# Optimization experiments

Measured on AMD Instinct MI355X. Metric: run time of the kernel, lower is better.

Reference implementation:

```python
import jax, jax.numpy as jnp
import numpy as np

EPS = 1e-5
NUM_HEADS = 8
KEY_DIM = 16
D = 64  # attn_ratio * key_dim


def conv1x1_bn(x, w, g, b, m, v):
    # x: (B, Cin, H, W), w: (Cout, Cin); eval-mode BatchNorm over channel dim
    y = jnp.einsum('bchw,oc->bohw', x, w)
    scale = (g * jax.lax.rsqrt(v + EPS))[None, :, None, None]
    shift = (b - g * m * jax.lax.rsqrt(v + EPS))[None, :, None, None]
    return y * scale + shift


def setup_inputs() -> dict:
    key = jax.random.key(0)
    ks = jax.random.split(key, 22)
    dim, nh_kd, dh = 384, 128, 512
    f = jax.random.normal
    u = jax.random.uniform
    return {
        'x': f(ks[0], (2, dim, 56, 56), jnp.float32),
        'wq': f(ks[1], (nh_kd, dim), jnp.float32) * 0.05,
        'qg': u(ks[2], (nh_kd,), jnp.float32), 'qb': f(ks[3], (nh_kd,)) * 0.1,
        'qm': f(ks[4], (nh_kd,)) * 0.1, 'qv': u(ks[5], (nh_kd,)) + 0.5,
        'wk': f(ks[6], (nh_kd, dim), jnp.float32) * 0.05,
        'kg': u(ks[7], (nh_kd,), jnp.float32), 'kb': f(ks[8], (nh_kd,)) * 0.1,
        'km': f(ks[9], (nh_kd,)) * 0.1, 'kvv': u(ks[10], (nh_kd,)) + 0.5,
        'wv': f(ks[11], (dh, dim), jnp.float32) * 0.05,
        'vg': u(ks[12], (dh,), jnp.float32), 'vb': f(ks[13], (dh,)) * 0.1,
        'vm': f(ks[14], (dh,)) * 0.1, 'vvv': u(ks[15], (dh,)) + 0.5,
        'wp': f(ks[16], (dim, dh), jnp.float32) * 0.05,
        'pg': u(ks[17], (dim,), jnp.float32), 'pb': f(ks[18], (dim,)) * 0.1,
        'pm': f(ks[19], (dim,)) * 0.1, 'pvv': u(ks[20], (dim,)) + 0.5,
    }


def reference(x, wq, qg, qb, qm, qv, wk, kg, kb, km, kvv,
              wv, vg, vb, vm, vvv, wp, pg, pb, pm, pvv):
    B, C, H, W = x.shape
    N = H * W
    h, kd, d = NUM_HEADS, KEY_DIM, D
    # (B, h, N, kd)
    qq = conv1x1_bn(x, wq, qg, qb, qm, qv).reshape(B, h, kd, N).transpose(0, 1, 3, 2)
    # (B, h, kd, N)
    kk = conv1x1_bn(x, wk, kg, kb, km, kvv).reshape(B, h, kd, N)
    # (B, h, N, d)
    vv = conv1x1_bn(x, wv, vg, vb, vm, vvv).reshape(B, h, d, N).transpose(0, 1, 3, 2)
    # NOTE: original forward does NOT apply self.scale
    attn = jax.nn.softmax(jnp.matmul(qq, kk), axis=-1)  # (B, h, N, N)
    xx = jnp.matmul(attn, vv)                            # (B, h, N, d)
    xx = xx.transpose(0, 1, 3, 2).reshape(B, h * d, H, W)
    xx = jax.nn.relu(xx)
    return conv1x1_bn(xx, wp, pg, pb, pm, pvv)
```

## Files before the change

kernel.cpp:

```cpp
#include <hip/hip_runtime.h>
#include <hip/hip_bf16.h>

#define B_   2
#define CIN  384
#define NPIX 3136
#define NH   8
#define KD   16
#define DHEAD 64
#define NHKD 128
#define QKW  256
#define DHD  512
#define EPSW 1e-5f

typedef __attribute__((ext_vector_type(8))) short vshort8;
typedef __attribute__((ext_vector_type(4))) short vshort4;
typedef __attribute__((ext_vector_type(4))) float vfloat4;
typedef __attribute__((ext_vector_type(16))) float vfloat16;

static __device__ __forceinline__ float bf2f(short s) {
    unsigned int u = ((unsigned int)(unsigned short)s) << 16;
    return __builtin_bit_cast(float, u);
}
static __device__ __forceinline__ short f2bf(float f) {
    unsigned int u = __builtin_bit_cast(unsigned int, f);
    unsigned int lsb = (u >> 16) & 1u;
    u += 0x7fffu + lsb;
    return (short)(u >> 16);
}
static __device__ __forceinline__ float pget(const void* p, int i, int f32) {
    return f32 ? ((const float*)p)[i] : bf2f(((const short*)p)[i]);
}

static __device__ __forceinline__ int detect_f32(const unsigned short* x) {
    int lane = threadIdx.x & 63;
    bool big = false;
#pragma unroll
    for (int j = 0; j < 8; j++) {
        int e = (x[(lane * 8 + j) * 2] >> 7) & 0xFF;
        big = big || (e >= 0xC0);
    }
    unsigned long long bal = __ballot(big);
    return __popcll(bal) >= 32;
}

__global__ __launch_bounds__(256) void prep_kernel(
    const void* __restrict__ x,
    const void* __restrict__ wq, const void* __restrict__ wk,
    const void* __restrict__ wv, const void* __restrict__ wp,
    short* __restrict__ wB, short* __restrict__ xT,
    const void* qg, const void* qb, const void* qm, const void* qv,
    const void* kg, const void* kb, const void* km, const void* kv,
    const void* vg, const void* vb, const void* vm, const void* vv,
    const void* pg, const void* pb, const void* pm, const void* pv,
    float* __restrict__ scA, float* __restrict__ shA)
{
    __shared__ short tile[32][33];
    int f32 = detect_f32((const unsigned short*)x);
    int id = blockIdx.x;
    int t = threadIdx.x;

    if (id < 1920) {
        int i = id * 256 + t;
        const void* src; int j;
        if (i < 49152)       { src = wq; j = i; }
        else if (i < 98304)  { src = wk; j = i - 49152; }
        else if (i < 294912) { src = wv; j = i - 98304; }
        else                 { src = wp; j = i - 294912; }
        wB[i] = f32 ? f2bf(((const float*)src)[j]) : ((const short*)src)[j];
        if (i < 1152) {
            const void *g, *bb, *mn, *vr;
            if (i < 128)      { g = qg; bb = qb; mn = qm; vr = qv; j = i; }
            else if (i < 256) { g = kg; bb = kb; mn = km; vr = kv; j = i - 128; }
            else if (i < 768) { g = vg; bb = vb; mn = vm; vr = vv; j = i - 256; }
            else              { g = pg; bb = pb; mn = pm; vr = pv; j = i - 768; }
            float iv = rsqrtf(pget(vr, j, f32) + EPSW);
            float s = pget(g, j, f32) * iv;
            scA[i] = s;
            shA[i] = pget(bb, j, f32) - pget(mn, j, f32) * s;
        }
        return;
    }

    int tid2 = id - 1920;
    int b = tid2 / 1176, rr = tid2 % 1176;
    int n0 = (rr % 98) * 32, c0 = (rr / 98) * 32;
    int r = t >> 3, q4 = (t & 7) * 4;
    size_t off = ((size_t)b * CIN + c0 + r) * NPIX + n0 + q4;
    if (f32) {
        float4 v = *(const float4*)((const float*)x + off);
        tile[r][q4 + 0] = f2bf(v.x);
        tile[r][q4 + 1] = f2bf(v.y);
        tile[r][q4 + 2] = f2bf(v.z);
        tile[r][q4 + 3] = f2bf(v.w);
    } else {
        vshort4 v = *(const vshort4*)((const short*)x + off);
#pragma unroll
        for (int i = 0; i < 4; i++) tile[r][q4 + i] = v[i];
    }
    __syncthreads();
    vshort4 o;
#pragma unroll
    for (int i = 0; i < 4; i++) o[i] = tile[q4 + i][r];
    *(vshort4*)(xT + ((size_t)b * NPIX + n0 + r) * CIN + c0 + q4) = o;
}

static __device__ __forceinline__ void gemm_body(
    short* Al, short* Bl,
    const short* __restrict__ A, const short* __restrict__ Bt,
    void* __restrict__ C, size_t coff, int m0, int n0,
    const float* __restrict__ sc, const float* __restrict__ sh,
    int Nb, int K, int bnPerRow, int finalOut, int f32)
{
    int t = threadIdx.x, lane = t & 63, w = t >> 6, m = lane & 15, quad = lane >> 4;
    int srow = t >> 2, scol = (t & 3) * 16;
    const short* ag = A + (size_t)(m0 + srow) * K + scol;
    const short* bg = Bt + (size_t)(n0 + srow) * K + scol;
    vfloat4 acc[4];
#pragma unroll
    for (int i = 0; i < 4; i++) acc[i] = (vfloat4){0.f, 0.f, 0.f, 0.f};

    for (int k0 = 0; k0 < K; k0 += 64) {
        vshort8 a0 = *(const vshort8*)(ag + k0);
        vshort8 a1 = *(const vshort8*)(ag + k0 + 8);
        vshort8 b0 = *(const vshort8*)(bg + k0);
        vshort8 b1 = *(const vshort8*)(bg + k0 + 8);
        __syncthreads();
        *(vshort8*)&Al[srow * 72 + scol] = a0;
        *(vshort8*)&Al[srow * 72 + scol + 8] = a1;
        *(vshort8*)&Bl[srow * 72 + scol] = b0;
        *(vshort8*)&Bl[srow * 72 + scol + 8] = b1;
        __syncthreads();
#pragma unroll
        for (int kk = 0; kk < 2; kk++) {
            vshort8 af = *(const vshort8*)&Al[(w * 16 + m) * 72 + kk * 32 + quad * 8];
#pragma unroll
            for (int nc = 0; nc < 4; nc++) {
                vshort8 bf = *(const vshort8*)&Bl[(nc * 16 + m) * 72 + kk * 32 + quad * 8];
                acc[nc] = __builtin_amdgcn_mfma_f32_16x16x32_bf16(af, bf, acc[nc], 0, 0, 0);
            }
        }
    }

#pragma unroll
    for (int nc = 0; nc < 4; nc++) {
        int col = n0 + nc * 16 + m;
        float scc = bnPerRow ? 0.f : sc[col];
        float shc = bnPerRow ? 0.f : sh[col];
#pragma unroll
        for (int r = 0; r < 4; r++) {
            int row = m0 + w * 16 + quad * 4 + r;
            float s2 = bnPerRow ? sc[row] : scc;
            float h2 = bnPerRow ? sh[row] : shc;
            float val = s2 * acc[nc][r] + h2;
            size_t idx = coff + (size_t)row * Nb + col;
            if (finalOut && f32) ((float*)C)[idx] = val;
            else                 ((short*)C)[idx] = f2bf(val);
        }
    }
}

__global__ __launch_bounds__(256) void proj_kernel(
    const short* __restrict__ xT, const short* __restrict__ wqkB,
    const short* __restrict__ wvB, short* __restrict__ QKt,
    short* __restrict__ Vb,
    const float* __restrict__ scA, const float* __restrict__ shA)
{
    __shared__ __attribute__((aligned(16))) short Al[64 * 72];
    __shared__ __attribute__((aligned(16))) short Bl[64 * 72];
    int id = blockIdx.x;
    if (id < 392) {
        int b = id / 196, r = id % 196;
        int m0 = (r % 49) * 64, n0 = (r / 49) * 64;
        gemm_body(Al, Bl, xT + (size_t)b * NPIX * CIN, wqkB,
                  QKt, (size_t)b * NPIX * QKW, m0, n0,
                  scA, shA, QKW, CIN, 0, 0, 0);
    } else {
        id -= 392;
        int b = id / 392, r = id % 392;
        int m0 = (r % 8) * 64, n0 = (r / 8) * 64;
        gemm_body(Al, Bl, wvB, xT + (size_t)b * NPIX * CIN,
                  Vb, (size_t)b * DHD * NPIX, m0, n0,
                  scA + 256, shA + 256, NPIX, CIN, 1, 0, 0);
    }
}

__global__ __launch_bounds__(256) void pgemm_kernel(
    const short* __restrict__ wpB, const short* __restrict__ xx,
    void* __restrict__ out,
    const float* __restrict__ scA, const float* __restrict__ shA,
    const void* __restrict__ x)
{
    __shared__ __attribute__((aligned(16))) short Al[64 * 72];
    __shared__ __attribute__((aligned(16))) short Bl[64 * 72];
    int f32 = detect_f32((const unsigned short*)x);
    int id = blockIdx.x;
    int b = id / 294, r = id % 294;
    int m0 = (r % 6) * 64, n0 = (r / 6) * 64;
    gemm_body(Al, Bl, wpB, xx + (size_t)b * NPIX * DHD,
              out, (size_t)b * CIN * NPIX, m0, n0,
              scA + 768, shA + 768, NPIX, DHD, 1, 1, f32);
}

__global__ __launch_bounds__(128) void attn_kernel(
    const short* __restrict__ QKt, const short* __restrict__ V,
    short* __restrict__ xx)
{
    __shared__ __attribute__((aligned(16))) short Kl[2][64 * 16];
    __shared__ __attribute__((aligned(16))) short Vl[2][64 * 72];
    __shared__ __attribute__((aligned(16))) short Pl[64 * 72];
    int bh = blockIdx.y, b = bh >> 3, h = bh & 7;
    int q0 = blockIdx.x * 64;
    int t = threadIdx.x, lane = t & 63, w = t >> 6;
    int c31 = lane & 31, half = lane >> 5;

    int q = q0 + w * 32 + c31;
    vshort8 aq = *(const vshort8*)(QKt + ((size_t)b * NPIX + q) * QKW + h * KD + half * 8);

    vfloat16 o0, o1, oL, z16;
#pragma unroll
    for (int i = 0; i < 16; i++) { o0[i] = 0.f; o1[i] = 0.f; oL[i] = 0.f; z16[i] = 0.f; }

    int kkey = t >> 1, kofs = (t & 1) * 8;
    const short* kgp = QKt + (size_t)b * NPIX * QKW + NHKD + h * KD + kofs;
    int vd = t >> 1, vkh = (t & 1) * 32;
    const short* vgp = V + ((size_t)(b * DHD) + h * DHEAD + vd) * NPIX + vkh;
    const short one_bf = (short)0x3F80;
    const vshort8 ones = {one_bf, one_bf, one_bf, one_bf, one_bf, one_bf, one_bf, one_bf};

    *(vshort8*)&Kl[0][kkey * 16 + kofs] = *(const vshort8*)(kgp + (size_t)kkey * QKW);
#pragma unroll
    for (int i = 0; i < 4; i++)
        *(vshort8*)&Vl[0][vd * 72 + vkh + i * 8] = *(const vshort8*)(vgp + i * 8);
    __syncthreads();

    for (int it = 0; it < NPIX / 64; ++it) {
        int cur = it & 1, nxt = cur ^ 1;
        int k0 = it * 64;
        bool more = (it + 1) < (NPIX / 64);
        vshort8 ks, vs[4];
        if (more) {
            ks = *(const vshort8*)(kgp + (size_t)(k0 + 64 + kkey) * QKW);
#pragma unroll
            for (int i = 0; i < 4; i++)
                vs[i] = *(const vshort8*)(vgp + k0 + 64 + i * 8);
        }

        short* pw = &Pl[(w * 32 + c31) * 72];
#pragma unroll
        for (int kg = 0; kg < 2; kg++) {
            vshort8 ak = *(const vshort8*)&Kl[cur][(kg * 32 + c31) * 16 + half * 8];
            vfloat16 s = __builtin_amdgcn_mfma_f32_32x32x16_bf16(ak, aq, z16, 0, 0, 0);
#pragma unroll
            for (int rb = 0; rb < 4; rb++) {
                vshort4 pv;
#pragma unroll
                for (int j = 0; j < 4; j++) {
                    float p = __expf(s[rb * 4 + j]);
                    pv[j] = (short)(__builtin_bit_cast(unsigned int, p) >> 16);
                }
                *(vshort4*)&pw[kg * 32 + half * 4 + rb * 8] = pv;
            }
        }

#pragma unroll
        for (int kc = 0; kc < 4; kc++) {
            vshort8 ap  = *(const vshort8*)&Pl[(w * 32 + c31) * 72 + kc * 16 + half * 8];
            vshort8 bv0 = *(const vshort8*)&Vl[cur][(c31) * 72 + kc * 16 + half * 8];
            vshort8 bv1 = *(const vshort8*)&Vl[cur][(32 + c31) * 72 + kc * 16 + half * 8];
            o0 = __builtin_amdgcn_mfma_f32_32x32x16_bf16(ap, bv0, o0, 0, 0, 0);
            o1 = __builtin_amdgcn_mfma_f32_32x32x16_bf16(ap, bv1, o1, 0, 0, 0);
            oL = __builtin_amdgcn_mfma_f32_32x32x16_bf16(ap, ones, oL, 0, 0, 0);
        }

        if (more) {
            *(vshort8*)&Kl[nxt][kkey * 16 + kofs] = ks;
#pragma unroll
            for (int i = 0; i < 4; i++)
                *(vshort8*)&Vl[nxt][vd * 72 + vkh + i * 8] = vs[i];
        }
        __syncthreads();
    }

#pragma unroll
    for (int r = 0; r < 16; r++) {
        int ql = (r & 3) + 8 * (r >> 2) + 4 * half;
        int qrow = q0 + w * 32 + ql;
        float inv = 1.0f / oL[r];
        size_t base = ((size_t)b * NPIX + qrow) * DHD + h * DHEAD + c31;
        xx[base]      = f2bf(fmaxf(o0[r] * inv, 0.f));
        xx[base + 32] = f2bf(fmaxf(o1[r] * inv, 0.f));
    }
}

extern "C" void kernel_launch(void* const* d_in, const int* in_sizes, int n_in,
                              void* d_out, int out_size, void* d_ws, size_t ws_size,
                              hipStream_t stream) {
    const void* x  = d_in[0];
    const void* wq = d_in[1];
    const void* qg = d_in[2];  const void* qb = d_in[3];
    const void* qm = d_in[4];  const void* qv = d_in[5];
    const void* wk = d_in[6];
    const void* kg = d_in[7];  const void* kb = d_in[8];
    const void* km = d_in[9];  const void* kv = d_in[10];
    const void* wv = d_in[11];
    const void* vg = d_in[12]; const void* vb = d_in[13];
    const void* vm = d_in[14]; const void* vv = d_in[15];
    const void* wp = d_in[16];
    const void* pg = d_in[17]; const void* pb = d_in[18];
    const void* pm = d_in[19]; const void* pv = d_in[20];

    short* xT  = (short*)d_ws;
    short* wB  = xT + (size_t)B_ * NPIX * CIN;
    short* wqkB = wB;
    short* wvB  = wB + 98304;
    short* wpB  = wB + 294912;
    short* QKt = wB + 491520;
    short* Vb  = QKt + (size_t)B_ * NPIX * QKW;
    short* xx  = Vb + (size_t)B_ * DHD * NPIX;
    float* scA = (float*)(xx + (size_t)B_ * NPIX * DHD);
    float* shA = scA + 1152;

    prep_kernel<<<4272, 256, 0, stream>>>(
        x, wq, wk, wv, wp, wB, xT,
        qg, qb, qm, qv, kg, kb, km, kv,
        vg, vb, vm, vv, pg, pb, pm, pv, scA, shA);

    proj_kernel<<<1176, 256, 0, stream>>>(xT, wqkB, wvB, QKt, Vb, scA, shA);

    attn_kernel<<<dim3(NPIX / 64, B_ * NH), 128, 0, stream>>>(QKt, Vb, xx);

    pgemm_kernel<<<588, 256, 0, stream>>>(wpB, xx, d_out, scA, shA, x);
}
```

Baseline: 197.2 us.

## Retile projection GEMMs to 128x64 with 32x32 MFMA and fold log2e into Q

```diff
diff --git a/kernel.cpp b/kernel.cpp
--- a/kernel.cpp
+++ b/kernel.cpp
@@ -11,11 +11,18 @@
 #define QKW  256
 #define DHD  512
 #define EPSW 1e-5f
+#define L2E  1.4426950408889634f
 
 typedef __attribute__((ext_vector_type(8))) short vshort8;
 typedef __attribute__((ext_vector_type(4))) short vshort4;
 typedef __attribute__((ext_vector_type(4))) float vfloat4;
 typedef __attribute__((ext_vector_type(16))) float vfloat16;
+
+#if __has_builtin(__builtin_amdgcn_exp2f)
+#define EXP2F __builtin_amdgcn_exp2f
+#else
+#define EXP2F exp2f
+#endif
 
 static __device__ __forceinline__ float bf2f(short s) {
     unsigned int u = ((unsigned int)(unsigned short)s) << 16;
@@ -75,8 +82,10 @@
             else              { g = pg; bb = pb; mn = pm; vr = pv; j = i - 768; }
             float iv = rsqrtf(pget(vr, j, f32) + EPSW);
             float s = pget(g, j, f32) * iv;
+            float h = pget(bb, j, f32) - pget(mn, j, f32) * s;
+            if (i < 128) { s *= L2E; h *= L2E; }
             scA[i] = s;
-            shA[i] = pget(bb, j, f32) - pget(mn, j, f32) * s;
+            shA[i] = h;
         }
         return;
     }
@@ -104,54 +113,63 @@
     *(vshort4*)(xT + ((size_t)b * NPIX + n0 + r) * CIN + c0 + q4) = o;
 }
 
-static __device__ __forceinline__ void gemm_body(
+static __device__ __forceinline__ void gemm32_body(
     short* Al, short* Bl,
     const short* __restrict__ A, const short* __restrict__ Bt,
     void* __restrict__ C, size_t coff, int m0, int n0,
     const float* __restrict__ sc, const float* __restrict__ sh,
-    int Nb, int K, int bnPerRow, int finalOut, int f32)
-{
-    int t = threadIdx.x, lane = t & 63, w = t >> 6, m = lane & 15, quad = lane >> 4;
-    int srow = t >> 2, scol = (t & 3) * 16;
-    const short* ag = A + (size_t)(m0 + srow) * K + scol;
-    const short* bg = Bt + (size_t)(n0 + srow) * K + scol;
-    vfloat4 acc[4];
-#pragma unroll
-    for (int i = 0; i < 4; i++) acc[i] = (vfloat4){0.f, 0.f, 0.f, 0.f};
+    int Nb, int K, int Mreal, int bnPerRow, int finalOut, int f32)
+{
+    int t = threadIdx.x, lane = t & 63, w = t >> 6;
+    int c31 = lane & 31, half = lane >> 5;
+    int arow = t >> 1, ak = (t & 1) * 32;
+    int brow = t >> 2, bk = (t & 3) * 16;
+    const short* ag = A + (size_t)(m0 + arow) * K + ak;
+    const short* bg = Bt + (size_t)(n0 + brow) * K + bk;
+
+    vfloat16 acc0, acc1;
+#pragma unroll
+    for (int i = 0; i < 16; i++) { acc0[i] = 0.f; acc1[i] = 0.f; }
 
     for (int k0 = 0; k0 < K; k0 += 64) {
         vshort8 a0 = *(const vshort8*)(ag + k0);
         vshort8 a1 = *(const vshort8*)(ag + k0 + 8);
+        vshort8 a2 = *(const vshort8*)(ag + k0 + 16);
+        vshort8 a3 = *(const vshort8*)(ag + k0 + 24);
         vshort8 b0 = *(const vshort8*)(bg + k0);
         vshort8 b1 = *(const vshort8*)(bg + k0 + 8);
         __syncthreads();
-        *(vshort8*)&Al[srow * 72 + scol] = a0;
-        *(vshort8*)&Al[srow * 72 + scol + 8] = a1;
-        *(vshort8*)&Bl[srow * 72 + scol] = b0;
-        *(vshort8*)&Bl[srow * 72 + scol + 8] = b1;
+        *(vshort8*)&Al[arow * 72 + ak]      = a0;
+        *(vshort8*)&Al[arow * 72 + ak + 8]  = a1;
+        *(vshort8*)&Al[arow * 72 + ak + 16] = a2;
+        *(vshort8*)&Al[arow * 72 + ak + 24] = a3;
+        *(vshort8*)&Bl[brow * 72 + bk]      = b0;
+        *(vshort8*)&Bl[brow * 72 + bk + 8]  = b1;
         __syncthreads();
 #pragma unroll
-        for (int kk = 0; kk < 2; kk++) {
-            vshort8 af = *(const vshort8*)&Al[(w * 16 + m) * 72 + kk * 32 + quad * 8];
-#pragma unroll
-            for (int nc = 0; nc < 4; nc++) {
-                vshort8 bf = *(const vshort8*)&Bl[(nc * 16 + m) * 72 + kk * 32 + quad * 8];
-                acc[nc] = __builtin_amdgcn_mfma_f32_16x16x32_bf16(af, bf, acc[nc], 0, 0, 0);
-            }
-        }
-    }
-
-#pragma unroll
-    for (int nc = 0; nc < 4; nc++) {
-        int col = n0 + nc * 16 + m;
+        for (int ks = 0; ks < 4; ks++) {
+            vshort8 af  = *(const vshort8*)&Al[(w * 32 + c31) * 72 + ks * 16 + half * 8];
+            vshort8 bf0 = *(const vshort8*)&Bl[(c31) * 72 + ks * 16 + half * 8];
+            vshort8 bf1 = *(const vshort8*)&Bl[(32 + c31) * 72 + ks * 16 + half * 8];
+            acc0 = __builtin_amdgcn_mfma_f32_32x32x16_bf16(af, bf0, acc0, 0, 0, 0);
+            acc1 = __builtin_amdgcn_mfma_f32_32x32x16_bf16(af, bf1, acc1, 0, 0, 0);
+        }
+    }
+
+#pragma unroll
+    for (int cb = 0; cb < 2; cb++) {
+        int col = n0 + cb * 32 + c31;
         float scc = bnPerRow ? 0.f : sc[col];
         float shc = bnPerRow ? 0.f : sh[col];
 #pragma unroll
-        for (int r = 0; r < 4; r++) {
-            int row = m0 + w * 16 + quad * 4 + r;
+        for (int r = 0; r < 16; r++) {
+            int rowl = (r & 3) + 8 * (r >> 2) + 4 * half;
+            int row = m0 + w * 32 + rowl;
+            if (row >= Mreal) continue;
             float s2 = bnPerRow ? sc[row] : scc;
             float h2 = bnPerRow ? sh[row] : shc;
-            float val = s2 * acc[nc][r] + h2;
+            float v = cb ? acc1[r] : acc0[r];
+            float val = s2 * v + h2;
             size_t idx = coff + (size_t)row * Nb + col;
             if (finalOut && f32) ((float*)C)[idx] = val;
             else                 ((short*)C)[idx] = f2bf(val);
@@ -165,22 +183,22 @@
     short* __restrict__ Vb,
     const float* __restrict__ scA, const float* __restrict__ shA)
 {
-    __shared__ __attribute__((aligned(16))) short Al[64 * 72];
+    __shared__ __attribute__((aligned(16))) short Al[128 * 72];
     __shared__ __attribute__((aligned(16))) short Bl[64 * 72];
     int id = blockIdx.x;
-    if (id < 392) {
+    if (id < 200) {
+        int b = id / 100, r = id % 100;
+        int m0 = (r % 25) * 128, n0 = (r / 25) * 64;
+        gemm32_body(Al, Bl, xT + (size_t)b * NPIX * CIN, wqkB,
+                    QKt, (size_t)b * NPIX * QKW, m0, n0,
+                    scA, shA, QKW, CIN, NPIX, 0, 0, 0);
+    } else {
+        id -= 200;
         int b = id / 196, r = id % 196;
-        int m0 = (r % 49) * 64, n0 = (r / 49) * 64;
-        gemm_body(Al, Bl, xT + (size_t)b * NPIX * CIN, wqkB,
-                  QKt, (size_t)b * NPIX * QKW, m0, n0,
-                  scA, shA, QKW, CIN, 0, 0, 0);
-    } else {
-        id -= 392;
-        int b = id / 392, r = id % 392;
-        int m0 = (r % 8) * 64, n0 = (r / 8) * 64;
-        gemm_body(Al, Bl, wvB, xT + (size_t)b * NPIX * CIN,
-                  Vb, (size_t)b * DHD * NPIX, m0, n0,
-                  scA + 256, shA + 256, NPIX, CIN, 1, 0, 0);
+        int m0 = (r / 49) * 128, n0 = (r % 49) * 64;
+        gemm32_body(Al, Bl, wvB, xT + (size_t)b * NPIX * CIN,
+                    Vb, (size_t)b * DHD * NPIX, m0, n0,
+                    scA + 256, shA + 256, NPIX, CIN, DHD, 1, 0, 0);
     }
 }
 
@@ -190,15 +208,15 @@
     const float* __restrict__ scA, const float* __restrict__ shA,
     const void* __restrict__ x)
 {
-    __shared__ __attribute__((aligned(16))) short Al[64 * 72];
+    __shared__ __attribute__((aligned(16))) short Al[128 * 72];
     __shared__ __attribute__((aligned(16))) short Bl[64 * 72];
     int f32 = detect_f32((const unsigned short*)x);
     int id = blockIdx.x;
-    int b = id / 294, r = id % 294;
-    int m0 = (r % 6) * 64, n0 = (r / 6) * 64;
-    gemm_body(Al, Bl, wpB, xx + (size_t)b * NPIX * DHD,
-              out, (size_t)b * CIN * NPIX, m0, n0,
-              scA + 768, shA + 768, NPIX, DHD, 1, 1, f32);
+    int b = id / 147, r = id % 147;
+    int m0 = (r / 49) * 128, n0 = (r % 49) * 64;
+    gemm32_body(Al, Bl, wpB, xx + (size_t)b * NPIX * DHD,
+                out, (size_t)b * CIN * NPIX, m0, n0,
+                scA + 768, shA + 768, NPIX, DHD, CIN, 1, 1, f32);
 }
 
 __global__ __launch_bounds__(128) void attn_kernel(
@@ -255,7 +273,7 @@
                 vshort4 pv;
 #pragma unroll
                 for (int j = 0; j < 4; j++) {
-                    float p = __expf(s[rb * 4 + j]);
+                    float p = EXP2F(s[rb * 4 + j]);
                     pv[j] = (short)(__builtin_bit_cast(unsigned int, p) >> 16);
                 }
                 *(vshort4*)&pw[kg * 32 + half * 4 + rb * 8] = pv;
@@ -325,9 +343,9 @@
         qg, qb, qm, qv, kg, kb, km, kv,
         vg, vb, vm, vv, pg, pb, pm, pv, scA, shA);
 
-    proj_kernel<<<1176, 256, 0, stream>>>(xT, wqkB, wvB, QKt, Vb, scA, shA);
+    proj_kernel<<<592, 256, 0, stream>>>(xT, wqkB, wvB, QKt, Vb, scA, shA);
 
     attn_kernel<<<dim3(NPIX / 64, B_ * NH), 128, 0, stream>>>(QKt, Vb, xx);
 
-    pgemm_kernel<<<588, 256, 0, stream>>>(wpB, xx, d_out, scA, shA, x);
-}
+    pgemm_kernel<<<294, 256, 0, stream>>>(wpB, xx, d_out, scA, shA, x);
+}
```

Measured after the change: 199.5 us. Within noise of the previous version (+1.1%).
